# Kernel tuning notes

Measured on AMD Instinct MI355X. Metric: run time of the kernel, lower is better.

The kernel has to match this reference:

```python
import jax, jax.numpy as jnp
import numpy as np

K = 9    # temporal kernel_size
V = 25   # graph vertices (joints)
P = 2    # persons


def setup_inputs() -> dict:
    key = jax.random.key(0)
    k1, k2, k3 = jax.random.split(key, 3)
    B, T, A, C, F, N = 8, 300, 3, 64, 64, 4
    data_batch = jax.random.normal(k1, (B, T, A, V * P, C), dtype=jnp.float32)
    kernel = jax.random.normal(k2, (N, K, F, C), dtype=jnp.float32) * 0.05
    neighbors = jax.random.randint(k3, (V, N), 0, V, dtype=jnp.int32)
    return {"data_batch": data_batch, "kernel": kernel, "neighbors": neighbors}


def reference(data_batch, kernel, neighbors):
    # data_batch: (B, T, A, V*P, C); kernel: (N, K, F, C); neighbors: (V, N)
    B, T, A, VP, C = data_batch.shape
    F = kernel.shape[2]
    Tt = T - K + 1  # valid temporal length
    x = data_batch.reshape(B, T, A, V, P, C)  # split joints/persons (vertex-major)
    # neighbor_matrix: matrix[k,f,c,u,v] = sum_n kernel[n,k,f,c] * 1[v == n-th neighbor of u]
    oh = jax.nn.one_hot(neighbors, V, dtype=kernel.dtype)        # (V_u, N, V_v)
    matrix = jnp.einsum('nkfc,unv->kfcuv', kernel, oh)            # (K, F, C, V, V)
    # valid temporal conv + graph contraction; loop over small fixed K avoids
    # materializing the K-fold tilted tensor the original builds via pad/slice/stack
    out = jnp.zeros((B, Tt, A, V, P, F), dtype=data_batch.dtype)
    for k in range(K):
        out = out + jnp.einsum('btavpc,fcuv->btaupf', x[:, k:k + Tt], matrix[k])
    out = out.reshape(B, Tt, A, V * P, F)
    # padding='same': original pads kernel_size-1 zeros at the END of time
    out = jnp.pad(out, ((0, 0), (0, K - 1), (0, 0), (0, 0), (0, 0)))
    return out  # activation=None -> identity
```

## Files before the change

### kernel.cpp

```cpp
#include <hip/hip_runtime.h>
#include <hip/hip_bf16.h>

typedef __attribute__((ext_vector_type(8))) short short8;
typedef __attribute__((ext_vector_type(4))) float f32x4;
typedef __attribute__((ext_vector_type(2))) unsigned int u32x2;
typedef __attribute__((ext_vector_type(4))) unsigned int u32x4;

#define SLAB 9216

__device__ __forceinline__ unsigned sw(unsigned off) {
  return off ^ (((off >> 7) & 3u) << 4);
}

__device__ __forceinline__ unsigned pk2(float lo, float hi) {
  union { __hip_bfloat162 h; unsigned u; } c;
  c.h = __float22bfloat162_rn(float2{lo, hi});
  return c.u;
}

extern "C" __global__ void w_prep(const float* __restrict__ ker, u32x4* __restrict__ wsw) {
  const int nk = blockIdx.x % 36;
  const int ch = blockIdx.x / 36;
  const int lane = threadIdx.x & 63;
  const int ft = threadIdx.x >> 6;
  const float* src = ker + (size_t)(nk * 64 + ft * 16 + (lane & 15)) * 64
                         + ch * 32 + (lane >> 4) * 8;
  f32x4 a0 = *(const f32x4*)src;
  f32x4 a1 = *(const f32x4*)(src + 4);
  u32x4 h = { pk2(a0.x, a0.y), pk2(a0.z, a0.w), pk2(a1.x, a1.y), pk2(a1.z, a1.w) };
  wsw[((ch * 36 + nk) * 4 + ft) * 64 + lane] = h;
}

#define KSTEP(KK, WREG, S2, K2, PF) do {                                       \
    const int _wo = (((S2) & 1) * 9216) + (((S2) >> 1) * 2304) + ((K2) * 256) + fhl; \
    short8 _n0 = wqb[_wo];                                                     \
    short8 _n1 = wqb[_wo + 64];                                                \
    if (PF) {                                                                  \
      const unsigned _kq = cb + (unsigned)(((((KK) + 1)) >> 2) * 512) + poff[((KK) + 1) & 3]; \
      bnxt0 = *(const short8*)(xs + _kq);                                      \
      bnxt1 = *(const short8*)(xs + _kq + 1024u);                              \
      bnxt2 = *(const short8*)(xs + _kq + 2048u);                              \
      bnxt3 = *(const short8*)(xs + _kq + 3072u);                              \
    }                                                                          \
    __builtin_amdgcn_s_setprio(1);                                             \
    acc[0][0] = __builtin_amdgcn_mfma_f32_16x16x32_bf16(WREG[0], bcur0, acc[0][0], 0, 0, 0); \
    acc[1][0] = __builtin_amdgcn_mfma_f32_16x16x32_bf16(WREG[1], bcur0, acc[1][0], 0, 0, 0); \
    acc[0][1] = __builtin_amdgcn_mfma_f32_16x16x32_bf16(WREG[0], bcur1, acc[0][1], 0, 0, 0); \
    acc[1][1] = __builtin_amdgcn_mfma_f32_16x16x32_bf16(WREG[1], bcur1, acc[1][1], 0, 0, 0); \
    acc[0][2] = __builtin_amdgcn_mfma_f32_16x16x32_bf16(WREG[0], bcur2, acc[0][2], 0, 0, 0); \
    acc[1][2] = __builtin_amdgcn_mfma_f32_16x16x32_bf16(WREG[1], bcur2, acc[1][2], 0, 0, 0); \
    acc[0][3] = __builtin_amdgcn_mfma_f32_16x16x32_bf16(WREG[0], bcur3, acc[0][3], 0, 0, 0); \
    acc[1][3] = __builtin_amdgcn_mfma_f32_16x16x32_bf16(WREG[1], bcur3, acc[1][3], 0, 0, 0); \
    __builtin_amdgcn_s_setprio(0);                                             \
    WREG[0] = _n0; WREG[1] = _n1;                                              \
    if (PF) { bcur0 = bnxt0; bcur1 = bnxt1; bcur2 = bnxt2; bcur3 = bnxt3; }    \
  } while (0)

extern "C" __global__ __launch_bounds__(256, 3)
void glc_mfma(const float* __restrict__ x, const short8* __restrict__ wsw,
              const int* __restrict__ nb, float* __restrict__ out) {
  __shared__ __align__(16) char xs[2 * SLAB];

  const int d = blockIdx.x;
  const int l = (d & 7) * 375 + (d >> 3);
  const int u  = l % 25;
  const int tt = (l / 25) % 5;
  const int a  = (l / 125) % 3;
  const int b  = l / 375;
  const int t0 = tt * 64;

  const int tid  = threadIdx.x;
  const int lane = tid & 63;
  const int wave = tid >> 6;
  const int fhalf = wave >> 1;
  const int tq   = wave & 1;
  const int fhl  = fhalf * 128;

  const int rl = lane & 15, gq = lane >> 4;
  unsigned poff[4];
#pragma unroll
  for (int m = 0; m < 4; ++m)
    poff[m] = sw((unsigned)((2 * m + rl) * 64 + gq * 16));

  f32x4 acc[2][4];
#pragma unroll
  for (int j = 0; j < 2; ++j)
#pragma unroll
    for (int i = 0; i < 4; ++i) acc[j][i] = (f32x4){0.f, 0.f, 0.f, 0.f};

  int goff[5];
#pragma unroll
  for (int j = 0; j < 5; ++j) {
    const int idx = j * 256 + tid;
    const int r = idx >> 3;
    const int q = idx & 7;
    int t = t0 + (r >> 1); if (t > 299) t = 299;
    goff[j] = t * 9600 + (r & 1) * 64 + q * 4;
  }
  const float* xb = x + (size_t)b * (300 * 9600) + (size_t)a * 3200;
  const short8* wqb = wsw + lane;
  const int* nbu = nb + u * 4;

  f32x4 sr[5];
  auto stage_load = [&](int snx) {
    const int add = nbu[snx >> 1] * 128 + (snx & 1) * 32;
#pragma unroll
    for (int j = 0; j < 5; ++j)
      if (j < 4 || tid < 128)
        sr[j] = *(const f32x4*)(xb + goff[j] + add);
  };
  auto stage_write = [&](int snx) {
    char* dst = xs + (snx & 1) * SLAB;
#pragma unroll
    for (int j = 0; j < 5; ++j)
      if (j < 4 || tid < 128) {
        const int idx = j * 256 + tid;
        const int r = idx >> 3, q = idx & 7;
        u32x2 h = { pk2(sr[j].x, sr[j].y), pk2(sr[j].z, sr[j].w) };
        *(u32x2*)(dst + sw((unsigned)(r * 64 + q * 8))) = h;
      }
  };

  short8 wA[2], wB[2], wC[2];
  {
    const int o0 = 0 * 256 + fhl, o1 = 1 * 256 + fhl, o2 = 2 * 256 + fhl;
    wA[0] = wqb[o0]; wA[1] = wqb[o0 + 64];
    wB[0] = wqb[o1]; wB[1] = wqb[o1 + 64];
    wC[0] = wqb[o2]; wC[1] = wqb[o2 + 64];
  }
  stage_load(0);
  stage_write(0);
  __syncthreads();

  short8 bcur0, bcur1, bcur2, bcur3;
  short8 bnxt0, bnxt1, bnxt2, bnxt3;

#pragma unroll 1
  for (int s = 0; s < 8; ++s) {
    const int sn = (s < 7) ? (s + 1) : 7;
    const unsigned cb = (unsigned)((s & 1) * SLAB + tq * 4096);
    {
      const unsigned kq0 = cb + poff[0];
      bcur0 = *(const short8*)(xs + kq0);
      bcur1 = *(const short8*)(xs + kq0 + 1024u);
      bcur2 = *(const short8*)(xs + kq0 + 2048u);
      bcur3 = *(const short8*)(xs + kq0 + 3072u);
    }
    if (s < 7) stage_load(s + 1);
    KSTEP(0, wA, s, 3, 1);  KSTEP(1, wB, s, 4, 1);  KSTEP(2, wC, s, 5, 1);
    KSTEP(3, wA, s, 6, 1);  KSTEP(4, wB, s, 7, 1);  KSTEP(5, wC, s, 8, 1);
    KSTEP(6, wA, sn, 0, 1); KSTEP(7, wB, sn, 1, 1); KSTEP(8, wC, sn, 2, 0);
    if (s < 7) {
      stage_write(s + 1);
      __syncthreads();
    }
  }

  const int fb = fhalf * 32 + gq * 4;
  const f32x4 z4 = (f32x4){0.f, 0.f, 0.f, 0.f};
#pragma unroll
  for (int i = 0; i < 4; ++i) {
    const int col = (tq * 4 + i) * 16 + rl;
    const int t = t0 + (col >> 1);
    const int p = col & 1;
    if (t < 300) {
      float* dst = out + ((size_t)((b * 300 + t) * 3 + a) * 50 + (u * 2 + p)) * 64 + fb;
      const bool valid = (t < 292);
#pragma unroll
      for (int j = 0; j < 2; ++j) {
        f32x4 v = valid ? acc[j][i] : z4;
        __builtin_nontemporal_store(v, (f32x4*)(dst + j * 16));
      }
    }
  }
}

extern "C" void kernel_launch(void* const* d_in, const int* in_sizes, int n_in,
                              void* d_out, int out_size, void* d_ws, size_t ws_size,
                              hipStream_t stream) {
  const float* x   = (const float*)d_in[0];
  const float* ker = (const float*)d_in[1];
  const int*   nb  = (const int*)d_in[2];
  float* out = (float*)d_out;

  w_prep<<<dim3(72), dim3(256), 0, stream>>>(ker, (u32x4*)d_ws);
  glc_mfma<<<dim3(3000), dim3(256), 0, stream>>>(x, (const short8*)d_ws, nb, out);
}
```

Baseline: 113.8 us.

## Process two stages per barrier with doubled LDS buffer

Restructures the main loop from 8 iterations of one stage each into 4 iterations that each process two stages, with each LDS parity buffer holding two slabs. This halves the number of __syncthreads barriers. Global loads for the next two stages are split and interleaved with the MFMA steps. The cost is double the shared memory per block (about 36 KB), which may reduce how many blocks fit per CU.

```diff
diff --git a/kernel.cpp b/kernel.cpp
--- a/kernel.cpp
+++ b/kernel.cpp
@@ -7,6 +7,7 @@
 typedef __attribute__((ext_vector_type(4))) unsigned int u32x4;
 
 #define SLAB 9216
+#define BUF  18432
 
 __device__ __forceinline__ unsigned sw(unsigned off) {
   return off ^ (((off >> 7) & 3u) << 4);
@@ -31,12 +32,12 @@
   wsw[((ch * 36 + nk) * 4 + ft) * 64 + lane] = h;
 }
 
-#define KSTEP(KK, WREG, S2, K2, PF) do {                                       \
-    const int _wo = (((S2) & 1) * 9216) + (((S2) >> 1) * 2304) + ((K2) * 256) + fhl; \
+#define KSTEP(WREG, NKT, CBP, KP, PF) do {                                     \
+    const int _wo = (NKT) * 256 + fhl;                                         \
     short8 _n0 = wqb[_wo];                                                     \
     short8 _n1 = wqb[_wo + 64];                                                \
     if (PF) {                                                                  \
-      const unsigned _kq = cb + (unsigned)(((((KK) + 1)) >> 2) * 512) + poff[((KK) + 1) & 3]; \
+      const unsigned _kq = (CBP) + (unsigned)((((KP)) >> 2) * 512) + poff[(KP) & 3]; \
       bnxt0 = *(const short8*)(xs + _kq);                                      \
       bnxt1 = *(const short8*)(xs + _kq + 1024u);                              \
       bnxt2 = *(const short8*)(xs + _kq + 2048u);                              \
@@ -59,7 +60,7 @@
 extern "C" __global__ __launch_bounds__(256, 3)
 void glc_mfma(const float* __restrict__ x, const short8* __restrict__ wsw,
               const int* __restrict__ nb, float* __restrict__ out) {
-  __shared__ __align__(16) char xs[2 * SLAB];
+  __shared__ __align__(16) char xs[2 * BUF];
 
   const int d = blockIdx.x;
   const int l = (d & 7) * 375 + (d >> 3);
@@ -109,8 +110,8 @@
       if (j < 4 || tid < 128)
         sr[j] = *(const f32x4*)(xb + goff[j] + add);
   };
-  auto stage_write = [&](int snx) {
-    char* dst = xs + (snx & 1) * SLAB;
+  auto stage_write = [&](int par, int half) {
+    char* dst = xs + par * BUF + half * SLAB;
 #pragma unroll
     for (int j = 0; j < 5; ++j)
       if (j < 4 || tid < 128) {
@@ -123,35 +124,52 @@
 
   short8 wA[2], wB[2], wC[2];
   {
-    const int o0 = 0 * 256 + fhl, o1 = 1 * 256 + fhl, o2 = 2 * 256 + fhl;
-    wA[0] = wqb[o0]; wA[1] = wqb[o0 + 64];
-    wB[0] = wqb[o1]; wB[1] = wqb[o1 + 64];
-    wC[0] = wqb[o2]; wC[1] = wqb[o2 + 64];
+    wA[0] = wqb[0 * 256 + fhl]; wA[1] = wqb[0 * 256 + fhl + 64];
+    wB[0] = wqb[1 * 256 + fhl]; wB[1] = wqb[1 * 256 + fhl + 64];
+    wC[0] = wqb[2 * 256 + fhl]; wC[1] = wqb[2 * 256 + fhl + 64];
   }
   stage_load(0);
-  stage_write(0);
+  stage_write(0, 0);
+  stage_load(1);
+  stage_write(0, 1);
   __syncthreads();
 
   short8 bcur0, bcur1, bcur2, bcur3;
   short8 bnxt0, bnxt1, bnxt2, bnxt3;
 
 #pragma unroll 1
-  for (int s = 0; s < 8; ++s) {
-    const int sn = (s < 7) ? (s + 1) : 7;
-    const unsigned cb = (unsigned)((s & 1) * SLAB + tq * 4096);
+  for (int n = 0; n < 4; ++n) {
+    const bool last = (n == 3);
+    const unsigned cb0 = (unsigned)((n & 1) * BUF + tq * 4096);
+    const unsigned cb1 = cb0 + (unsigned)SLAB;
+    const int w0 = n * 9;
+    const int w1 = 36 + n * 9;
+    const int w2 = last ? 27 : (n + 1) * 9;
+
     {
-      const unsigned kq0 = cb + poff[0];
+      const unsigned kq0 = cb0 + poff[0];
       bcur0 = *(const short8*)(xs + kq0);
       bcur1 = *(const short8*)(xs + kq0 + 1024u);
       bcur2 = *(const short8*)(xs + kq0 + 2048u);
       bcur3 = *(const short8*)(xs + kq0 + 3072u);
     }
-    if (s < 7) stage_load(s + 1);
-    KSTEP(0, wA, s, 3, 1);  KSTEP(1, wB, s, 4, 1);  KSTEP(2, wC, s, 5, 1);
-    KSTEP(3, wA, s, 6, 1);  KSTEP(4, wB, s, 7, 1);  KSTEP(5, wC, s, 8, 1);
-    KSTEP(6, wA, sn, 0, 1); KSTEP(7, wB, sn, 1, 1); KSTEP(8, wC, sn, 2, 0);
-    if (s < 7) {
-      stage_write(s + 1);
+    if (!last) stage_load(2 * (n + 1));
+
+    KSTEP(wA, w0 + 3, cb0, 1, 1);  KSTEP(wB, w0 + 4, cb0, 2, 1);  KSTEP(wC, w0 + 5, cb0, 3, 1);
+    KSTEP(wA, w0 + 6, cb0, 4, 1);  KSTEP(wB, w0 + 7, cb0, 5, 1);  KSTEP(wC, w0 + 8, cb0, 6, 1);
+    KSTEP(wA, w1 + 0, cb0, 7, 1);  KSTEP(wB, w1 + 1, cb0, 8, 1);  KSTEP(wC, w1 + 2, cb1, 0, 1);
+
+    if (!last) {
+      stage_write((n + 1) & 1, 0);
+      stage_load(2 * (n + 1) + 1);
+    }
+
+    KSTEP(wA, w1 + 3, cb1, 1, 1);  KSTEP(wB, w1 + 4, cb1, 2, 1);  KSTEP(wC, w1 + 5, cb1, 3, 1);
+    KSTEP(wA, w1 + 6, cb1, 4, 1);  KSTEP(wB, w1 + 7, cb1, 5, 1);  KSTEP(wC, w1 + 8, cb1, 6, 1);
+    KSTEP(wA, w2 + 0, cb1, 7, 1);  KSTEP(wB, w2 + 1, cb1, 8, 1);  KSTEP(wC, w2 + 2, cb1, 8, 0);
+
+    if (!last) {
+      stage_write((n + 1) & 1, 1);
       __syncthreads();
     }
   }
```

Result: slower. 116.9 us (+2.7%).
